# Optimization experiments

Measured on AMD Instinct MI355X. Metric: run time of the kernel, lower is better.

Reference implementation:

```python
import jax, jax.numpy as jnp
import numpy as np

B, S, DQK, DV, H = 4, 2048, 128, 128, 8


def setup_inputs() -> dict:
    key = jax.random.key(0)
    ks = jax.random.split(key, 9)
    s = 0.02
    return {
        "query": jax.random.normal(ks[0], (B, S, DQK), jnp.float32),
        "key": jax.random.normal(ks[1], (B, S, DQK), jnp.float32),
        "value": jax.random.normal(ks[2], (B, S, DV), jnp.float32),
        "WQ": jax.random.normal(ks[3], (DQK, H * DQK), jnp.float32) * s,
        "bQ": jax.random.normal(ks[4], (H * DQK,), jnp.float32) * s,
        "WK": jax.random.normal(ks[5], (DQK, H * DQK), jnp.float32) * s,
        "bK": jax.random.normal(ks[6], (H * DQK,), jnp.float32) * s,
        "WV": jax.random.normal(ks[7], (DV, H * DV), jnp.float32) * s,
        "bV": jax.random.normal(ks[8], (H * DV,), jnp.float32) * s,
    }


def reference(query, key, value, WQ, bQ, WK, bK, WV, bV):
    b, qn, dqk = query.shape
    kn = key.shape[1]
    dv = value.shape[2]
    h = H
    # projections -> [b, n, h, d]
    Q = (query @ WQ + bQ).reshape(b, qn, h, dqk)
    K = (key @ WK + bK).reshape(b, kn, h, dqk)
    V = (value @ WV + bV).reshape(b, kn, h, dv)
    # abs(QK^T)/sqrt(dk) score -- non-standard, prevents flash kernels
    scores = jnp.abs(jnp.einsum("bqhd,bkhd->bhqk", Q, K)) / jnp.sqrt(
        jnp.asarray(dqk, query.dtype)
    )
    w = jax.nn.softmax(scores, axis=-1)  # [b,h,q,k]
    # (complex cast +0j in the original is numerically a no-op on real V)
    out = jnp.einsum("bhqk,bkhd->bqhd", w, V).reshape(b, qn, h * dv)
    return out
```

## Files before the change

kernel.cpp:

```cpp
#include <hip/hip_runtime.h>
#include <hip/hip_bf16.h>

#define B_ 4
#define S_ 2048
#define D_ 128
#define H_ 8

typedef __attribute__((ext_vector_type(8))) short bf16x8;
typedef __attribute__((ext_vector_type(4))) float f32x4;

__device__ __forceinline__ short f2bf(float f) {
  union { float f; unsigned u; } v; v.f = f;
  unsigned u = v.u;
  unsigned r = (u + 0x7FFFu + ((u >> 16) & 1u)) >> 16;
  return (short)r;
}

__device__ __forceinline__ short4 pack4(f32x4 p) {
  union { __hip_bfloat162 h2[2]; short4 s4; } u;
  u.h2[0] = __float22bfloat162_rn(make_float2(p[0], p[1]));
  u.h2[1] = __float22bfloat162_rn(make_float2(p[2], p[3]));
  return u.s4;
}

__device__ __forceinline__ void dma16(const short* g, short* l) {
  __builtin_amdgcn_global_load_lds(
      (const __attribute__((address_space(1))) unsigned int*)g,
      (__attribute__((address_space(3))) unsigned int*)l, 16, 0, 0);
}

__global__ __launch_bounds__(256) void prep(
    const float* __restrict__ WQ, const float* __restrict__ WK, const float* __restrict__ WV,
    short* __restrict__ FQ, short* __restrict__ FK, short* __restrict__ FV) {
  __shared__ float tile[64][65];
  int bw = blockIdx.x >> 5;
  int tl = blockIdx.x & 31;
  int n0 = (tl & 15) * 64, k0 = (tl >> 4) * 64;
  const float* W = (bw == 0) ? WQ : (bw == 1) ? WK : WV;
  short* WF = (bw == 0) ? FQ : (bw == 1) ? FK : FV;
#pragma unroll
  for (int i = 0; i < 16; ++i) {
    int cix = threadIdx.x + 256 * i;
    int rr = cix >> 6, cc = cix & 63;
    tile[rr][cc] = W[(k0 + rr) * 1024 + n0 + cc];
  }
  __syncthreads();
#pragma unroll
  for (int i = 0; i < 16; ++i) {
    int cix = threadIdx.x + 256 * i;
    int rr = cix >> 6, cc = cix & 63;
    int n = n0 + rr, k = k0 + cc;
    size_t off = (size_t)(n >> 7) * 16384
               + (size_t)(((n >> 4) & 7) * 4 + (k >> 5)) * 512
               + ((k >> 3) & 3) * 128 + (n & 15) * 8 + (k & 7);
    WF[off] = f2bf(tile[cc][rr]);
  }
}

template <int MODE>
__device__ __forceinline__ void proj_tile(const float* __restrict__ X,
                                          const short* __restrict__ WF,
                                          const float* __restrict__ bias,
                                          short* __restrict__ out,
                                          int mtile, int ntile,
                                          short* sA) {
  int tid = threadIdx.x;
  int lane = tid & 63, w = tid >> 6;
  int l15 = lane & 15, l4 = lane >> 4;
  int m0 = mtile * 128, n0 = ntile * 128;

#pragma unroll
  for (int j = 0; j < 8; ++j) {
    int f = w * 8 + j;
    const float* src = X + (size_t)(m0 + (f >> 2) * 16 + l15) * 128 + (f & 3) * 32 + l4 * 8;
    float4 v0 = *(const float4*)src;
    float4 v1 = *(const float4*)(src + 4);
    union { struct { short4 lo, hi; } s; bf16x8 v; } u;
    u.s.lo = pack4((f32x4){v0.x, v0.y, v0.z, v0.w});
    u.s.hi = pack4((f32x4){v1.x, v1.y, v1.z, v1.w});
    *(bf16x8*)(sA + f * 512 + lane * 8) = u.v;
  }

  int wr = w >> 1, wc = w & 1;

  const short* wfb = WF + (size_t)ntile * 16384 + wc * 8192 + lane * 8;
  bf16x8 b[16];
#pragma unroll
  for (int q = 0; q < 16; ++q)
    b[q] = *(const bf16x8*)(wfb + q * 512);

  __syncthreads();

  f32x4 acc[4][4];
#pragma unroll
  for (int mi = 0; mi < 4; ++mi)
#pragma unroll
    for (int ni = 0; ni < 4; ++ni) acc[mi][ni] = (f32x4){0.f, 0.f, 0.f, 0.f};

#pragma unroll
  for (int mi = 0; mi < 4; ++mi) {
    bf16x8 a[4];
#pragma unroll
    for (int st = 0; st < 4; ++st)
      a[st] = *(const bf16x8*)(sA + ((wr * 4 + mi) * 4 + st) * 512 + lane * 8);
#pragma unroll
    for (int ni = 0; ni < 4; ++ni) {
#pragma unroll
      for (int st = 0; st < 4; ++st) {
        if (MODE <= 1)
          acc[mi][ni] = __builtin_amdgcn_mfma_f32_16x16x32_bf16(b[ni * 4 + st], a[st], acc[mi][ni], 0, 0, 0);
        else
          acc[mi][ni] = __builtin_amdgcn_mfma_f32_16x16x32_bf16(a[st], b[ni * 4 + st], acc[mi][ni], 0, 0, 0);
      }
    }
  }

  if (MODE == 0) {
#pragma unroll
    for (int mi = 0; mi < 4; ++mi) {
      int sg = m0 + wr * 64 + mi * 16 + l15;
      int bb = sg >> 11, s = sg & 2047;
      short* orow = out + ((size_t)(bb * H_ + ntile) * S_ + s) * D_;
#pragma unroll
      for (int ni = 0; ni < 4; ++ni) {
        int d0 = wc * 64 + ni * 16 + l4 * 4;
        float4 bv = *(const float4*)(bias + n0 + d0);
        f32x4 t = acc[mi][ni];
        t[0] += bv.x; t[1] += bv.y; t[2] += bv.z; t[3] += bv.w;
        *(short4*)(orow + d0) = pack4(t);
      }
    }
  } else if (MODE == 1) {
#pragma unroll
    for (int mi = 0; mi < 4; ++mi) {
      int key = m0 + wr * 64 + mi * 16 + l15;
      int bb = key >> 11, k = key & 2047;
      size_t base = (size_t)(bb * H_ + ntile) * (S_ * D_) + (size_t)(k >> 6) * 8192
                  + ((k >> 4) & 3) * 4 * 512 + (k & 15) * 8;
#pragma unroll
      for (int ni = 0; ni < 4; ++ni) {
        int d0 = wc * 64 + ni * 16 + l4 * 4;
        float4 bv = *(const float4*)(bias + n0 + d0);
        f32x4 t = acc[mi][ni];
        t[0] += bv.x; t[1] += bv.y; t[2] += bv.z; t[3] += bv.w;
        size_t off = base + (size_t)(d0 >> 5) * 512 + ((d0 >> 3) & 3) * 128 + (d0 & 7);
        *(short4*)(out + off) = pack4(t);
      }
    }
  } else {
#pragma unroll
    for (int ni = 0; ni < 4; ++ni) {
      int d = wc * 64 + ni * 16 + l15;
      float bvs = bias[n0 + d];
#pragma unroll
      for (int mi = 0; mi < 4; ++mi) {
        int sg0 = m0 + wr * 64 + mi * 16 + l4 * 4;
        int bb = sg0 >> 11, s0 = sg0 & 2047;
        f32x4 t = acc[mi][ni];
        t[0] += bvs; t[1] += bvs; t[2] += bvs; t[3] += bvs;
        size_t off = (size_t)(bb * H_ + ntile) * (S_ * D_)
                   + (size_t)(s0 >> 6) * 8192
                   + (size_t)((d >> 4) * 2 + ((s0 >> 5) & 1)) * 512
                   + ((s0 >> 3) & 3) * 128 + (d & 15) * 8
                   + (s0 & 7);
        *(short4*)(out + off) = pack4(t);
      }
    }
  }
}

__global__ __launch_bounds__(256, 3) void proj3(
    const float* __restrict__ xq, const float* __restrict__ xk, const float* __restrict__ xv,
    const short* __restrict__ wtq, const short* __restrict__ wtk, const short* __restrict__ wtv,
    const float* __restrict__ bQ, const float* __restrict__ bK, const float* __restrict__ bV,
    short* __restrict__ Qp, short* __restrict__ Kf, short* __restrict__ Vf) {
  __shared__ short sA[16384];
  int work = (blockIdx.x & 7) * 192 + (blockIdx.x >> 3);
  int which = work >> 9;
  int t = work & 511;
  int mtile = t >> 3, ntile = t & 7;
  if (which == 0)      proj_tile<0>(xq, wtq, bQ, Qp, mtile, ntile, sA);
  else if (which == 1) proj_tile<1>(xk, wtk, bK, Kf, mtile, ntile, sA);
  else                 proj_tile<2>(xv, wtv, bV, Vf, mtile, ntile, sA);
}

#define PSTR 72

#define QK_H(KR)                                                               \
  _Pragma("unroll") for (int m = 0; m < 2; ++m) {                              \
    s0[m] = (f32x4){0.f, 0.f, 0.f, 0.f};                                       \
    s1[m] = (f32x4){0.f, 0.f, 0.f, 0.f};                                       \
    _Pragma("unroll") for (int st = 0; st < 4; ++st) {                         \
      s0[m] = __builtin_amdgcn_mfma_f32_16x16x32_bf16(KR[m * 4 + st], aq[0][st], s0[m], 0, 0, 0); \
      s1[m] = __builtin_amdgcn_mfma_f32_16x16x32_bf16(KR[m * 4 + st], aq[1][st], s1[m], 0, 0, 0); \
    }                                                                          \
  }

#define SM_H()                                                                 \
  _Pragma("unroll") for (int m = 0; m < 2; ++m) {                              \
    _Pragma("unroll") for (int r = 0; r < 4; ++r) {                            \
      float p = __builtin_amdgcn_exp2f(fabsf(s0[m][r]) * SC2);                 \
      ls0 += p;                                                                \
      s0[m][r] = p;                                                            \
    }                                                                          \
    *(short4*)(pw + l15 * PSTR + m * 16 + l4 * 4) = pack4(s0[m]);              \
  }                                                                            \
  ap0 = *(const bf16x8*)(pw + l15 * PSTR + l4 * 8);                            \
  _Pragma("unroll") for (int m = 0; m < 2; ++m) {                              \
    _Pragma("unroll") for (int r = 0; r < 4; ++r) {                            \
      float p = __builtin_amdgcn_exp2f(fabsf(s1[m][r]) * SC2);                 \
      ls1 += p;                                                                \
      s1[m][r] = p;                                                            \
    }                                                                          \
    *(short4*)(pw + l15 * PSTR + m * 16 + l4 * 4) = pack4(s1[m]);              \
  }                                                                            \
  ap1 = *(const bf16x8*)(pw + l15 * PSTR + l4 * 8);

#define PV_H()                                                                 \
  _Pragma("unroll") for (int t8 = 0; t8 < 8; ++t8) {                           \
    o0[t8] = __builtin_amdgcn_mfma_f32_16x16x32_bf16(ap0, bv[t8], o0[t8], 0, 0, 0); \
    o1[t8] = __builtin_amdgcn_mfma_f32_16x16x32_bf16(ap1, bv[t8], o1[t8], 0, 0, 0); \
  }

__global__ __launch_bounds__(512, 2) void attn(const short* __restrict__ Qp,
                                               const short* __restrict__ Kf,
                                               const short* __restrict__ Vf,
                                               float* __restrict__ out) {
  __shared__ short sK0[8192], sK1[8192];
  __shared__ short sV0[8192], sV1[8192];
  __shared__ short sP[8 * 16 * PSTR];

  int tid = threadIdx.x;
  int lane = tid & 63, w = tid >> 6;
  int xcd = blockIdx.x & 7;
  int idx = blockIdx.x >> 3;
  int bh  = xcd * 4 + (idx & 3);
  int qt  = idx >> 2;
  int q0  = qt * 256;
  int l15 = lane & 15, l4 = lane >> 4;

  const short* Qbase = Qp + (size_t)bh * S_ * D_;
  const short* kgs = Kf + (size_t)bh * S_ * D_ + 2 * w * 512 + lane * 8;
  const short* vgs = Vf + (size_t)bh * S_ * D_ + 2 * w * 512 + lane * 8;

  dma16(kgs,       sK0 + 2 * w * 512);
  dma16(kgs + 512, sK0 + (2 * w + 1) * 512);
  dma16(vgs,       sV0 + 2 * w * 512);
  dma16(vgs + 512, sV0 + (2 * w + 1) * 512);

  bf16x8 aq[2][4];
#pragma unroll
  for (int g = 0; g < 2; ++g)
#pragma unroll
    for (int st = 0; st < 4; ++st)
      aq[g][st] = *(const bf16x8*)(Qbase + (q0 + w * 32 + g * 16 + l15) * D_ + l4 * 8 + 32 * st);

  f32x4 o0[8], o1[8];
#pragma unroll
  for (int t = 0; t < 8; ++t) {
    o0[t] = (f32x4){0.f, 0.f, 0.f, 0.f};
    o1[t] = (f32x4){0.f, 0.f, 0.f, 0.f};
  }
  float ls0 = 0.f, ls1 = 0.f;

  const float SC2 = 0.127530637f;
  short* pw = sP + w * 16 * PSTR;

  __syncthreads();

  for (int t = 0; t < 32; ++t) {
    const short* sKc = (t & 1) ? sK1 : sK0;
    const short* sVc = (t & 1) ? sV1 : sV0;
    if (t < 31) {
      short* sKn = (t & 1) ? sK0 : sK1;
      short* sVn = (t & 1) ? sV0 : sV1;
      const short* kn = kgs + (size_t)(t + 1) * 8192;
      const short* vn = vgs + (size_t)(t + 1) * 8192;
      dma16(kn,       sKn + 2 * w * 512);
      dma16(kn + 512, sKn + (2 * w + 1) * 512);
      dma16(vn,       sVn + 2 * w * 512);
      dma16(vn + 512, sVn + (2 * w + 1) * 512);
    }
    bf16x8 kA[8], kB[8], bv[8];
#pragma unroll
    for (int j = 0; j < 8; ++j)
      kA[j] = *(const bf16x8*)(sKc + j * 512 + lane * 8);
#pragma unroll
    for (int j = 0; j < 8; ++j)
      kB[j] = *(const bf16x8*)(sKc + 4096 + j * 512 + lane * 8);
#pragma unroll
    for (int j = 0; j < 8; ++j)
      bv[j] = *(const bf16x8*)(sVc + (2 * j) * 512 + lane * 8);
    __builtin_amdgcn_sched_barrier(0);

    f32x4 s0[2], s1[2];
    bf16x8 ap0, ap1;
    __builtin_amdgcn_s_setprio(1);
    QK_H(kA);
    __builtin_amdgcn_s_setprio(0);
    SM_H();
    __builtin_amdgcn_s_setprio(1);
    PV_H();
    __builtin_amdgcn_s_setprio(0);
#pragma unroll
    for (int j = 0; j < 8; ++j)
      bv[j] = *(const bf16x8*)(sVc + (2 * j + 1) * 512 + lane * 8);
    __builtin_amdgcn_s_setprio(1);
    QK_H(kB);
    __builtin_amdgcn_s_setprio(0);
    SM_H();
    __builtin_amdgcn_s_setprio(1);
    PV_H();
    __builtin_amdgcn_s_setprio(0);
    __syncthreads();
  }

  ls0 += __shfl_xor(ls0, 16);
  ls0 += __shfl_xor(ls0, 32);
  ls1 += __shfl_xor(ls1, 16);
  ls1 += __shfl_xor(ls1, 32);
  float inv0[4], inv1[4];
#pragma unroll
  for (int r = 0; r < 4; ++r) {
    inv0[r] = 1.f / __shfl(ls0, l4 * 4 + r);
    inv1[r] = 1.f / __shfl(ls1, l4 * 4 + r);
  }

  int bb = bh >> 3, h = bh & 7;
#pragma unroll
  for (int t = 0; t < 8; ++t) {
#pragma unroll
    for (int r = 0; r < 4; ++r) {
      int qA = q0 + w * 32 + l4 * 4 + r;
      int qB = qA + 16;
      out[((size_t)(bb * S_ + qA)) * (H_ * D_) + h * D_ + t * 16 + l15] = o0[t][r] * inv0[r];
      out[((size_t)(bb * S_ + qB)) * (H_ * D_) + h * D_ + t * 16 + l15] = o1[t][r] * inv1[r];
    }
  }
}

extern "C" void kernel_launch(void* const* d_in, const int* in_sizes, int n_in,
                              void* d_out, int out_size, void* d_ws, size_t ws_size,
                              hipStream_t stream) {
  (void)in_sizes; (void)n_in; (void)out_size; (void)ws_size;
  const float* q  = (const float*)d_in[0];
  const float* k  = (const float*)d_in[1];
  const float* v  = (const float*)d_in[2];
  const float* WQ = (const float*)d_in[3];
  const float* bQ = (const float*)d_in[4];
  const float* WK = (const float*)d_in[5];
  const float* bK = (const float*)d_in[6];
  const float* WV = (const float*)d_in[7];
  const float* bV = (const float*)d_in[8];

  const int NW = D_ * H_ * D_;
  const int NP = B_ * H_ * S_ * D_;

  short* ws  = (short*)d_ws;
  short* wtq = ws;
  short* wtk = wtq + NW;
  short* wtv = wtk + NW;
  short* Qp  = wtv + NW;
  short* Kf  = Qp + NP;
  short* Vf  = Kf + NP;

  prep<<<96, 256, 0, stream>>>(WQ, WK, WV, wtq, wtk, wtv);

  proj3<<<1536, 256, 0, stream>>>(q, k, v, wtq, wtk, wtv, bQ, bK, bV, Qp, Kf, Vf);

  attn<<<256, 512, 0, stream>>>(Qp, Kf, Vf, (float*)d_out);
}
```

Before: 184.0 us.

## Load projection activations directly into registers with prefetch; split P scratch buffers

The projection kernel no longer stages the converted activation tile through shared memory behind a barrier. Each wave loads its own fp32 rows from global memory, converts them to bf16 in registers, and prefetches the next 16-row slice while the current one feeds the MFMAs. The launch-bounds occupancy hint of 3 blocks is removed. In the attention kernel the P scratch is split into two per-wave buffers, so both half-tiles are written before either is read back, which removes the write-read dependency between them at the cost of doubling that LDS allocation.

```diff
diff --git a/kernel.cpp b/kernel.cpp
--- a/kernel.cpp
+++ b/kernel.cpp
@@ -57,31 +57,51 @@
   }
 }
 
+#define PJ_STEP(CUR, NXT, MI, PREF)                                            \
+  {                                                                            \
+    if (PREF) {                                                                \
+      const float* xn = xb + ((MI) + 1) * 2048;                                \
+      _Pragma("unroll") for (int st = 0; st < 4; ++st) {                       \
+        NXT[st][0] = *(const float4*)(xn + st * 32);                           \
+        NXT[st][1] = *(const float4*)(xn + st * 32 + 4);                       \
+      }                                                                        \
+    }                                                                          \
+    bf16x8 a[4];                                                               \
+    _Pragma("unroll") for (int st = 0; st < 4; ++st) {                         \
+      union { struct { short4 lo, hi; } s; bf16x8 v; } u;                      \
+      u.s.lo = pack4((f32x4){CUR[st][0].x, CUR[st][0].y, CUR[st][0].z, CUR[st][0].w}); \
+      u.s.hi = pack4((f32x4){CUR[st][1].x, CUR[st][1].y, CUR[st][1].z, CUR[st][1].w}); \
+      a[st] = u.v;                                                             \
+    }                                                                          \
+    _Pragma("unroll") for (int ni = 0; ni < 4; ++ni) {                         \
+      _Pragma("unroll") for (int st = 0; st < 4; ++st) {                       \
+        if (MODE <= 1)                                                         \
+          acc[MI][ni] = __builtin_amdgcn_mfma_f32_16x16x32_bf16(b[ni * 4 + st], a[st], acc[MI][ni], 0, 0, 0); \
+        else                                                                   \
+          acc[MI][ni] = __builtin_amdgcn_mfma_f32_16x16x32_bf16(a[st], b[ni * 4 + st], acc[MI][ni], 0, 0, 0); \
+      }                                                                        \
+    }                                                                          \
+  }
+
 template <int MODE>
 __device__ __forceinline__ void proj_tile(const float* __restrict__ X,
                                           const short* __restrict__ WF,
                                           const float* __restrict__ bias,
                                           short* __restrict__ out,
-                                          int mtile, int ntile,
-                                          short* sA) {
+                                          int mtile, int ntile) {
   int tid = threadIdx.x;
   int lane = tid & 63, w = tid >> 6;
   int l15 = lane & 15, l4 = lane >> 4;
   int m0 = mtile * 128, n0 = ntile * 128;
-
-#pragma unroll
-  for (int j = 0; j < 8; ++j) {
-    int f = w * 8 + j;
-    const float* src = X + (size_t)(m0 + (f >> 2) * 16 + l15) * 128 + (f & 3) * 32 + l4 * 8;
-    float4 v0 = *(const float4*)src;
-    float4 v1 = *(const float4*)(src + 4);
-    union { struct { short4 lo, hi; } s; bf16x8 v; } u;
-    u.s.lo = pack4((f32x4){v0.x, v0.y, v0.z, v0.w});
-    u.s.hi = pack4((f32x4){v1.x, v1.y, v1.z, v1.w});
-    *(bf16x8*)(sA + f * 512 + lane * 8) = u.v;
-  }
-
   int wr = w >> 1, wc = w & 1;
+
+  const float* xb = X + (size_t)(m0 + wr * 64 + l15) * 128 + l4 * 8;
+  float4 pa[4][2], pb[4][2];
+#pragma unroll
+  for (int st = 0; st < 4; ++st) {
+    pa[st][0] = *(const float4*)(xb + st * 32);
+    pa[st][1] = *(const float4*)(xb + st * 32 + 4);
+  }
 
   const short* wfb = WF + (size_t)ntile * 16384 + wc * 8192 + lane * 8;
   bf16x8 b[16];
@@ -89,31 +109,16 @@
   for (int q = 0; q < 16; ++q)
     b[q] = *(const bf16x8*)(wfb + q * 512);
 
-  __syncthreads();
-
   f32x4 acc[4][4];
 #pragma unroll
   for (int mi = 0; mi < 4; ++mi)
 #pragma unroll
     for (int ni = 0; ni < 4; ++ni) acc[mi][ni] = (f32x4){0.f, 0.f, 0.f, 0.f};
 
-#pragma unroll
-  for (int mi = 0; mi < 4; ++mi) {
-    bf16x8 a[4];
-#pragma unroll
-    for (int st = 0; st < 4; ++st)
-      a[st] = *(const bf16x8*)(sA + ((wr * 4 + mi) * 4 + st) * 512 + lane * 8);
-#pragma unroll
-    for (int ni = 0; ni < 4; ++ni) {
-#pragma unroll
-      for (int st = 0; st < 4; ++st) {
-        if (MODE <= 1)
-          acc[mi][ni] = __builtin_amdgcn_mfma_f32_16x16x32_bf16(b[ni * 4 + st], a[st], acc[mi][ni], 0, 0, 0);
-        else
-          acc[mi][ni] = __builtin_amdgcn_mfma_f32_16x16x32_bf16(a[st], b[ni * 4 + st], acc[mi][ni], 0, 0, 0);
-      }
-    }
-  }
+  PJ_STEP(pa, pb, 0, true);
+  PJ_STEP(pb, pa, 1, true);
+  PJ_STEP(pa, pb, 2, true);
+  PJ_STEP(pb, pa, 3, false);
 
   if (MODE == 0) {
 #pragma unroll
@@ -169,19 +174,18 @@
   }
 }
 
-__global__ __launch_bounds__(256, 3) void proj3(
+__global__ __launch_bounds__(256) void proj3(
     const float* __restrict__ xq, const float* __restrict__ xk, const float* __restrict__ xv,
     const short* __restrict__ wtq, const short* __restrict__ wtk, const short* __restrict__ wtv,
     const float* __restrict__ bQ, const float* __restrict__ bK, const float* __restrict__ bV,
     short* __restrict__ Qp, short* __restrict__ Kf, short* __restrict__ Vf) {
-  __shared__ short sA[16384];
   int work = (blockIdx.x & 7) * 192 + (blockIdx.x >> 3);
   int which = work >> 9;
   int t = work & 511;
   int mtile = t >> 3, ntile = t & 7;
-  if (which == 0)      proj_tile<0>(xq, wtq, bQ, Qp, mtile, ntile, sA);
-  else if (which == 1) proj_tile<1>(xk, wtk, bK, Kf, mtile, ntile, sA);
-  else                 proj_tile<2>(xv, wtv, bV, Vf, mtile, ntile, sA);
+  if (which == 0)      proj_tile<0>(xq, wtq, bQ, Qp, mtile, ntile);
+  else if (which == 1) proj_tile<1>(xk, wtk, bK, Kf, mtile, ntile);
+  else                 proj_tile<2>(xv, wtv, bV, Vf, mtile, ntile);
 }
 
 #define PSTR 72
@@ -203,18 +207,18 @@
       ls0 += p;                                                                \
       s0[m][r] = p;                                                            \
     }                                                                          \
-    *(short4*)(pw + l15 * PSTR + m * 16 + l4 * 4) = pack4(s0[m]);              \
+    *(short4*)(pw0 + l15 * PSTR + m * 16 + l4 * 4) = pack4(s0[m]);             \
   }                                                                            \
-  ap0 = *(const bf16x8*)(pw + l15 * PSTR + l4 * 8);                            \
   _Pragma("unroll") for (int m = 0; m < 2; ++m) {                              \
     _Pragma("unroll") for (int r = 0; r < 4; ++r) {                            \
       float p = __builtin_amdgcn_exp2f(fabsf(s1[m][r]) * SC2);                 \
       ls1 += p;                                                                \
       s1[m][r] = p;                                                            \
     }                                                                          \
-    *(short4*)(pw + l15 * PSTR + m * 16 + l4 * 4) = pack4(s1[m]);              \
+    *(short4*)(pw1 + l15 * PSTR + m * 16 + l4 * 4) = pack4(s1[m]);             \
   }                                                                            \
-  ap1 = *(const bf16x8*)(pw + l15 * PSTR + l4 * 8);
+  ap0 = *(const bf16x8*)(pw0 + l15 * PSTR + l4 * 8);                           \
+  ap1 = *(const bf16x8*)(pw1 + l15 * PSTR + l4 * 8);
 
 #define PV_H()                                                                 \
   _Pragma("unroll") for (int t8 = 0; t8 < 8; ++t8) {                           \
@@ -228,7 +232,7 @@
                                                float* __restrict__ out) {
   __shared__ short sK0[8192], sK1[8192];
   __shared__ short sV0[8192], sV1[8192];
-  __shared__ short sP[8 * 16 * PSTR];
+  __shared__ short sP[16 * 16 * PSTR];
 
   int tid = threadIdx.x;
   int lane = tid & 63, w = tid >> 6;
@@ -264,7 +268,8 @@
   float ls0 = 0.f, ls1 = 0.f;
 
   const float SC2 = 0.127530637f;
-  short* pw = sP + w * 16 * PSTR;
+  short* pw0 = sP + w * 16 * PSTR;
+  short* pw1 = sP + (8 + w) * 16 * PSTR;
 
   __syncthreads();
 
```

New measurement: 191.0 us. 3.8% more time.

## Fuse weight prep, projections and attention into one cooperative kernel

Applied to the files above, without the earlier changes.

Replaces the three launches (weight convert/swizzle, projection GEMM, attention) with a single cooperative kernel of 256 blocks of 512 threads, separated by grid-wide syncs. Each block redoes its share of the projection work as smaller 64-row subtiles processed with 8 waves before running attention. The aim is to remove launch gaps and tail effects between the kernels. In exchange it adds two grid barriers, limits occupancy to one block per CU with a larger shared allocation, and runs the projection phase with a different tiling. It also gives each P-tile half its own shared buffer.

```diff
diff --git a/kernel.cpp b/kernel.cpp
--- a/kernel.cpp
+++ b/kernel.cpp
@@ -1,5 +1,8 @@
 #include <hip/hip_runtime.h>
 #include <hip/hip_bf16.h>
+#include <hip/hip_cooperative_groups.h>
+
+namespace cg = cooperative_groups;
 
 #define B_ 4
 #define S_ 2048
@@ -29,49 +32,20 @@
       (__attribute__((address_space(3))) unsigned int*)l, 16, 0, 0);
 }
 
-__global__ __launch_bounds__(256) void prep(
-    const float* __restrict__ WQ, const float* __restrict__ WK, const float* __restrict__ WV,
-    short* __restrict__ FQ, short* __restrict__ FK, short* __restrict__ FV) {
-  __shared__ float tile[64][65];
-  int bw = blockIdx.x >> 5;
-  int tl = blockIdx.x & 31;
-  int n0 = (tl & 15) * 64, k0 = (tl >> 4) * 64;
-  const float* W = (bw == 0) ? WQ : (bw == 1) ? WK : WV;
-  short* WF = (bw == 0) ? FQ : (bw == 1) ? FK : FV;
-#pragma unroll
-  for (int i = 0; i < 16; ++i) {
-    int cix = threadIdx.x + 256 * i;
-    int rr = cix >> 6, cc = cix & 63;
-    tile[rr][cc] = W[(k0 + rr) * 1024 + n0 + cc];
-  }
-  __syncthreads();
-#pragma unroll
-  for (int i = 0; i < 16; ++i) {
-    int cix = threadIdx.x + 256 * i;
-    int rr = cix >> 6, cc = cix & 63;
-    int n = n0 + rr, k = k0 + cc;
-    size_t off = (size_t)(n >> 7) * 16384
-               + (size_t)(((n >> 4) & 7) * 4 + (k >> 5)) * 512
-               + ((k >> 3) & 3) * 128 + (n & 15) * 8 + (k & 7);
-    WF[off] = f2bf(tile[cc][rr]);
-  }
-}
-
 template <int MODE>
-__device__ __forceinline__ void proj_tile(const float* __restrict__ X,
-                                          const short* __restrict__ WF,
-                                          const float* __restrict__ bias,
-                                          short* __restrict__ out,
-                                          int mtile, int ntile,
-                                          short* sA) {
+__device__ __forceinline__ void proj_tile8(const float* __restrict__ X,
+                                           const short* __restrict__ WF,
+                                           const float* __restrict__ bias,
+                                           short* __restrict__ outp,
+                                           int mtile, int ntile, short* sA) {
   int tid = threadIdx.x;
   int lane = tid & 63, w = tid >> 6;
   int l15 = lane & 15, l4 = lane >> 4;
   int m0 = mtile * 128, n0 = ntile * 128;
 
 #pragma unroll
-  for (int j = 0; j < 8; ++j) {
-    int f = w * 8 + j;
+  for (int j = 0; j < 4; ++j) {
+    int f = w * 4 + j;
     const float* src = X + (size_t)(m0 + (f >> 2) * 16 + l15) * 128 + (f & 3) * 32 + l4 * 8;
     float4 v0 = *(const float4*)src;
     float4 v1 = *(const float4*)(src + 4);
@@ -82,7 +56,6 @@
   }
 
   int wr = w >> 1, wc = w & 1;
-
   const short* wfb = WF + (size_t)ntile * 16384 + wc * 8192 + lane * 8;
   bf16x8 b[16];
 #pragma unroll
@@ -91,18 +64,18 @@
 
   __syncthreads();
 
-  f32x4 acc[4][4];
-#pragma unroll
-  for (int mi = 0; mi < 4; ++mi)
+  f32x4 acc[2][4];
+#pragma unroll
+  for (int mi = 0; mi < 2; ++mi)
 #pragma unroll
     for (int ni = 0; ni < 4; ++ni) acc[mi][ni] = (f32x4){0.f, 0.f, 0.f, 0.f};
 
 #pragma unroll
-  for (int mi = 0; mi < 4; ++mi) {
+  for (int mi = 0; mi < 2; ++mi) {
     bf16x8 a[4];
 #pragma unroll
     for (int st = 0; st < 4; ++st)
-      a[st] = *(const bf16x8*)(sA + ((wr * 4 + mi) * 4 + st) * 512 + lane * 8);
+      a[st] = *(const bf16x8*)(sA + ((wr * 2 + mi) * 4 + st) * 512 + lane * 8);
 #pragma unroll
     for (int ni = 0; ni < 4; ++ni) {
 #pragma unroll
@@ -114,13 +87,14 @@
       }
     }
   }
+  __syncthreads();
 
   if (MODE == 0) {
 #pragma unroll
-    for (int mi = 0; mi < 4; ++mi) {
-      int sg = m0 + wr * 64 + mi * 16 + l15;
-      int bb = sg >> 11, s = sg & 2047;
-      short* orow = out + ((size_t)(bb * H_ + ntile) * S_ + s) * D_;
+    for (int mi = 0; mi < 2; ++mi) {
+      int sg = m0 + wr * 32 + mi * 16 + l15;
+      int b2 = sg >> 11, s = sg & 2047;
+      short* orow = outp + ((size_t)(b2 * H_ + ntile) * S_ + s) * D_;
 #pragma unroll
       for (int ni = 0; ni < 4; ++ni) {
         int d0 = wc * 64 + ni * 16 + l4 * 4;
@@ -132,11 +106,11 @@
     }
   } else if (MODE == 1) {
 #pragma unroll
-    for (int mi = 0; mi < 4; ++mi) {
-      int key = m0 + wr * 64 + mi * 16 + l15;
-      int bb = key >> 11, k = key & 2047;
-      size_t base = (size_t)(bb * H_ + ntile) * (S_ * D_) + (size_t)(k >> 6) * 8192
-                  + ((k >> 4) & 3) * 4 * 512 + (k & 15) * 8;
+    for (int mi = 0; mi < 2; ++mi) {
+      int key = m0 + wr * 32 + mi * 16 + l15;
+      int b2 = key >> 11, kk = key & 2047;
+      size_t base = (size_t)(b2 * H_ + ntile) * (S_ * D_) + (size_t)(kk >> 6) * 8192
+                  + ((kk >> 4) & 3) * 2048 + (kk & 15) * 8;
 #pragma unroll
       for (int ni = 0; ni < 4; ++ni) {
         int d0 = wc * 64 + ni * 16 + l4 * 4;
@@ -144,7 +118,7 @@
         f32x4 t = acc[mi][ni];
         t[0] += bv.x; t[1] += bv.y; t[2] += bv.z; t[3] += bv.w;
         size_t off = base + (size_t)(d0 >> 5) * 512 + ((d0 >> 3) & 3) * 128 + (d0 & 7);
-        *(short4*)(out + off) = pack4(t);
+        *(short4*)(outp + off) = pack4(t);
       }
     }
   } else {
@@ -153,35 +127,20 @@
       int d = wc * 64 + ni * 16 + l15;
       float bvs = bias[n0 + d];
 #pragma unroll
-      for (int mi = 0; mi < 4; ++mi) {
-        int sg0 = m0 + wr * 64 + mi * 16 + l4 * 4;
-        int bb = sg0 >> 11, s0 = sg0 & 2047;
+      for (int mi = 0; mi < 2; ++mi) {
+        int sg0 = m0 + wr * 32 + mi * 16 + l4 * 4;
+        int b2 = sg0 >> 11, s0 = sg0 & 2047;
         f32x4 t = acc[mi][ni];
         t[0] += bvs; t[1] += bvs; t[2] += bvs; t[3] += bvs;
-        size_t off = (size_t)(bb * H_ + ntile) * (S_ * D_)
+        size_t off = (size_t)(b2 * H_ + ntile) * (S_ * D_)
                    + (size_t)(s0 >> 6) * 8192
                    + (size_t)((d >> 4) * 2 + ((s0 >> 5) & 1)) * 512
                    + ((s0 >> 3) & 3) * 128 + (d & 15) * 8
                    + (s0 & 7);
-        *(short4*)(out + off) = pack4(t);
+        *(short4*)(outp + off) = pack4(t);
       }
     }
   }
-}
-
-__global__ __launch_bounds__(256, 3) void proj3(
-    const float* __restrict__ xq, const float* __restrict__ xk, const float* __restrict__ xv,
-    const short* __restrict__ wtq, const short* __restrict__ wtk, const short* __restrict__ wtv,
-    const float* __restrict__ bQ, const float* __restrict__ bK, const float* __restrict__ bV,
-    short* __restrict__ Qp, short* __restrict__ Kf, short* __restrict__ Vf) {
-  __shared__ short sA[16384];
-  int work = (blockIdx.x & 7) * 192 + (blockIdx.x >> 3);
-  int which = work >> 9;
-  int t = work & 511;
-  int mtile = t >> 3, ntile = t & 7;
-  if (which == 0)      proj_tile<0>(xq, wtq, bQ, Qp, mtile, ntile, sA);
-  else if (which == 1) proj_tile<1>(xk, wtk, bK, Kf, mtile, ntile, sA);
-  else                 proj_tile<2>(xv, wtv, bV, Vf, mtile, ntile, sA);
 }
 
 #define PSTR 72
@@ -203,18 +162,18 @@
       ls0 += p;                                                                \
       s0[m][r] = p;                                                            \
     }                                                                          \
-    *(short4*)(pw + l15 * PSTR + m * 16 + l4 * 4) = pack4(s0[m]);              \
+    *(short4*)(pw0 + l15 * PSTR + m * 16 + l4 * 4) = pack4(s0[m]);             \
   }                                                                            \
-  ap0 = *(const bf16x8*)(pw + l15 * PSTR + l4 * 8);                            \
   _Pragma("unroll") for (int m = 0; m < 2; ++m) {                              \
     _Pragma("unroll") for (int r = 0; r < 4; ++r) {                            \
       float p = __builtin_amdgcn_exp2f(fabsf(s1[m][r]) * SC2);                 \
       ls1 += p;                                                                \
       s1[m][r] = p;                                                            \
     }                                                                          \
-    *(short4*)(pw + l15 * PSTR + m * 16 + l4 * 4) = pack4(s1[m]);              \
+    *(short4*)(pw1 + l15 * PSTR + m * 16 + l4 * 4) = pack4(s1[m]);             \
   }                                                                            \
-  ap1 = *(const bf16x8*)(pw + l15 * PSTR + l4 * 8);
+  ap0 = *(const bf16x8*)(pw0 + l15 * PSTR + l4 * 8);                           \
+  ap1 = *(const bf16x8*)(pw1 + l15 * PSTR + l4 * 8);
 
 #define PV_H()                                                                 \
   _Pragma("unroll") for (int t8 = 0; t8 < 8; ++t8) {                           \
@@ -222,22 +181,69 @@
     o1[t8] = __builtin_amdgcn_mfma_f32_16x16x32_bf16(ap1, bv[t8], o1[t8], 0, 0, 0); \
   }
 
-__global__ __launch_bounds__(512, 2) void attn(const short* __restrict__ Qp,
-                                               const short* __restrict__ Kf,
-                                               const short* __restrict__ Vf,
-                                               float* __restrict__ out) {
-  __shared__ short sK0[8192], sK1[8192];
-  __shared__ short sV0[8192], sV1[8192];
-  __shared__ short sP[8 * 16 * PSTR];
+__global__ __launch_bounds__(512, 1) void fused(
+    const float* __restrict__ xq, const float* __restrict__ xk, const float* __restrict__ xv,
+    const float* __restrict__ WQ, const float* __restrict__ WK, const float* __restrict__ WV,
+    const float* __restrict__ bQ, const float* __restrict__ bK, const float* __restrict__ bV,
+    short* __restrict__ wfq, short* __restrict__ wfk, short* __restrict__ wfv,
+    short* __restrict__ Qp, short* __restrict__ Kf, short* __restrict__ Vf,
+    float* __restrict__ out) {
+  __shared__ short smem[51200];
 
   int tid = threadIdx.x;
   int lane = tid & 63, w = tid >> 6;
+  int l15 = lane & 15, l4 = lane >> 4;
   int xcd = blockIdx.x & 7;
   int idx = blockIdx.x >> 3;
   int bh  = xcd * 4 + (idx & 3);
   int qt  = idx >> 2;
-  int q0  = qt * 256;
-  int l15 = lane & 15, l4 = lane >> 4;
+  int bb  = bh >> 3, h = bh & 7;
+
+  if (blockIdx.x < 96) {
+    float* tile = (float*)smem;
+    int bw = blockIdx.x >> 5, tl = blockIdx.x & 31;
+    int n0 = (tl & 15) * 64, k0 = (tl >> 4) * 64;
+    const float* W = (bw == 0) ? WQ : (bw == 1) ? WK : WV;
+    short* WF = (bw == 0) ? wfq : (bw == 1) ? wfk : wfv;
+#pragma unroll
+    for (int i = 0; i < 8; ++i) {
+      int cix = tid + 512 * i;
+      int rr = cix >> 6, cc = cix & 63;
+      tile[rr * 65 + cc] = W[(k0 + rr) * 1024 + n0 + cc];
+    }
+    __syncthreads();
+#pragma unroll
+    for (int i = 0; i < 8; ++i) {
+      int cix = tid + 512 * i;
+      int rr = cix >> 6, cc = cix & 63;
+      int n = n0 + rr, k = k0 + cc;
+      size_t off = (size_t)(n >> 7) * 16384
+                 + (size_t)(((n >> 4) & 7) * 4 + (k >> 5)) * 512
+                 + ((k >> 3) & 3) * 128 + (n & 15) * 8 + (k & 7);
+      WF[off] = f2bf(tile[cc * 65 + rr]);
+    }
+  }
+  cg::this_grid().sync();
+
+  {
+    short* sA = smem;
+    int mt0 = bb * 16 + qt * 2;
+    proj_tile8<0>(xq, wfq, bQ, Qp, mt0,     h, sA);
+    proj_tile8<0>(xq, wfq, bQ, Qp, mt0 + 1, h, sA);
+    proj_tile8<1>(xk, wfk, bK, Kf, mt0,     h, sA);
+    proj_tile8<1>(xk, wfk, bK, Kf, mt0 + 1, h, sA);
+    proj_tile8<2>(xv, wfv, bV, Vf, mt0,     h, sA);
+    proj_tile8<2>(xv, wfv, bV, Vf, mt0 + 1, h, sA);
+  }
+  cg::this_grid().sync();
+
+  short* sK0 = smem;
+  short* sK1 = smem + 8192;
+  short* sV0 = smem + 16384;
+  short* sV1 = smem + 24576;
+  short* sP  = smem + 32768;
+
+  int q0 = qt * 256;
 
   const short* Qbase = Qp + (size_t)bh * S_ * D_;
   const short* kgs = Kf + (size_t)bh * S_ * D_ + 2 * w * 512 + lane * 8;
@@ -264,7 +270,8 @@
   float ls0 = 0.f, ls1 = 0.f;
 
   const float SC2 = 0.127530637f;
-  short* pw = sP + w * 16 * PSTR;
+  short* pw0 = sP + w * 16 * PSTR;
+  short* pw1 = sP + (8 + w) * 16 * PSTR;
 
   __syncthreads();
 
@@ -326,7 +333,6 @@
     inv1[r] = 1.f / __shfl(ls1, l4 * 4 + r);
   }
 
-  int bb = bh >> 3, h = bh & 7;
 #pragma unroll
   for (int t = 0; t < 8; ++t) {
 #pragma unroll
@@ -357,16 +363,21 @@
   const int NP = B_ * H_ * S_ * D_;
 
   short* ws  = (short*)d_ws;
-  short* wtq = ws;
-  short* wtk = wtq + NW;
-  short* wtv = wtk + NW;
-  short* Qp  = wtv + NW;
+  short* wfq = ws;
+  short* wfk = wfq + NW;
+  short* wfv = wfk + NW;
+  short* Qp  = wfv + NW;
   short* Kf  = Qp + NP;
   short* Vf  = Kf + NP;
-
-  prep<<<96, 256, 0, stream>>>(WQ, WK, WV, wtq, wtk, wtv);
-
-  proj3<<<1536, 256, 0, stream>>>(q, k, v, wtq, wtk, wtv, bQ, bK, bV, Qp, Kf, Vf);
-
-  attn<<<256, 512, 0, stream>>>(Qp, Kf, Vf, (float*)d_out);
-}
+  float* outp = (float*)d_out;
+
+  void* args[] = {
+    (void*)&q, (void*)&k, (void*)&v,
+    (void*)&WQ, (void*)&WK, (void*)&WV,
+    (void*)&bQ, (void*)&bK, (void*)&bV,
+    (void*)&wfq, (void*)&wfk, (void*)&wfv,
+    (void*)&Qp, (void*)&Kf, (void*)&Vf,
+    (void*)&outp,
+  };
+  hipLaunchCooperativeKernel((void*)fused, dim3(256), dim3(512), args, 0, stream);
+}
```

Result: slower. 254.7 us (+38.5%).

## Compute two output column tiles per projection block and double-buffer P scratch

Applied to the files above, without the earlier changes.

Each projection block now loads and converts one 128-row input tile, keeps its A fragments in registers, and computes two adjacent 128-column output tiles. This halves the grid and the redundant fp32 input loads and bf16 conversions, at the cost of more registers held per thread. In the attention kernel, the two 16-row P tiles per wave now get separate LDS scratch regions. Both tiles are written before either is read back, removing the write-read dependency between them, at the cost of doubling the sP LDS footprint.

```diff
diff --git a/kernel.cpp b/kernel.cpp
--- a/kernel.cpp
+++ b/kernel.cpp
@@ -58,16 +58,15 @@
 }
 
 template <int MODE>
-__device__ __forceinline__ void proj_tile(const float* __restrict__ X,
+__device__ __forceinline__ void proj_pair(const float* __restrict__ X,
                                           const short* __restrict__ WF,
                                           const float* __restrict__ bias,
                                           short* __restrict__ out,
-                                          int mtile, int ntile,
-                                          short* sA) {
+                                          int mtile, int np, short* sA) {
   int tid = threadIdx.x;
   int lane = tid & 63, w = tid >> 6;
   int l15 = lane & 15, l4 = lane >> 4;
-  int m0 = mtile * 128, n0 = ntile * 128;
+  int m0 = mtile * 128;
 
 #pragma unroll
   for (int j = 0; j < 8; ++j) {
@@ -83,87 +82,96 @@
 
   int wr = w >> 1, wc = w & 1;
 
-  const short* wfb = WF + (size_t)ntile * 16384 + wc * 8192 + lane * 8;
-  bf16x8 b[16];
-#pragma unroll
-  for (int q = 0; q < 16; ++q)
-    b[q] = *(const bf16x8*)(wfb + q * 512);
-
   __syncthreads();
 
-  f32x4 acc[4][4];
+  bf16x8 a[4][4];
 #pragma unroll
   for (int mi = 0; mi < 4; ++mi)
 #pragma unroll
-    for (int ni = 0; ni < 4; ++ni) acc[mi][ni] = (f32x4){0.f, 0.f, 0.f, 0.f};
-
-#pragma unroll
-  for (int mi = 0; mi < 4; ++mi) {
-    bf16x8 a[4];
-#pragma unroll
     for (int st = 0; st < 4; ++st)
-      a[st] = *(const bf16x8*)(sA + ((wr * 4 + mi) * 4 + st) * 512 + lane * 8);
-#pragma unroll
-    for (int ni = 0; ni < 4; ++ni) {
-#pragma unroll
-      for (int st = 0; st < 4; ++st) {
-        if (MODE <= 1)
-          acc[mi][ni] = __builtin_amdgcn_mfma_f32_16x16x32_bf16(b[ni * 4 + st], a[st], acc[mi][ni], 0, 0, 0);
-        else
-          acc[mi][ni] = __builtin_amdgcn_mfma_f32_16x16x32_bf16(a[st], b[ni * 4 + st], acc[mi][ni], 0, 0, 0);
+      a[mi][st] = *(const bf16x8*)(sA + ((wr * 4 + mi) * 4 + st) * 512 + lane * 8);
+
+#pragma unroll
+  for (int nt = 0; nt < 2; ++nt) {
+    int ntile = np * 2 + nt;
+    int n0 = ntile * 128;
+
+    const short* wfb = WF + (size_t)ntile * 16384 + wc * 8192 + lane * 8;
+    bf16x8 b[16];
+#pragma unroll
+    for (int q = 0; q < 16; ++q)
+      b[q] = *(const bf16x8*)(wfb + q * 512);
+
+    f32x4 acc[4][4];
+#pragma unroll
+    for (int mi = 0; mi < 4; ++mi)
+#pragma unroll
+      for (int ni = 0; ni < 4; ++ni) acc[mi][ni] = (f32x4){0.f, 0.f, 0.f, 0.f};
+
+#pragma unroll
+    for (int mi = 0; mi < 4; ++mi) {
+#pragma unroll
+      for (int ni = 0; ni < 4; ++ni) {
+#pragma unroll
+        for (int st = 0; st < 4; ++st) {
+          if (MODE <= 1)
+            acc[mi][ni] = __builtin_amdgcn_mfma_f32_16x16x32_bf16(b[ni * 4 + st], a[mi][st], acc[mi][ni], 0, 0, 0);
+          else
+            acc[mi][ni] = __builtin_amdgcn_mfma_f32_16x16x32_bf16(a[mi][st], b[ni * 4 + st], acc[mi][ni], 0, 0, 0);
+        }
       }
     }
-  }
-
-  if (MODE == 0) {
-#pragma unroll
-    for (int mi = 0; mi < 4; ++mi) {
-      int sg = m0 + wr * 64 + mi * 16 + l15;
-      int bb = sg >> 11, s = sg & 2047;
-      short* orow = out + ((size_t)(bb * H_ + ntile) * S_ + s) * D_;
+
+    if (MODE == 0) {
+#pragma unroll
+      for (int mi = 0; mi < 4; ++mi) {
+        int sg = m0 + wr * 64 + mi * 16 + l15;
+        int bb = sg >> 11, s = sg & 2047;
+        short* orow = out + ((size_t)(bb * H_ + ntile) * S_ + s) * D_;
+#pragma unroll
+        for (int ni = 0; ni < 4; ++ni) {
+          int d0 = wc * 64 + ni * 16 + l4 * 4;
+          float4 bv = *(const float4*)(bias + n0 + d0);
+          f32x4 t = acc[mi][ni];
+          t[0] += bv.x; t[1] += bv.y; t[2] += bv.z; t[3] += bv.w;
+          *(short4*)(orow + d0) = pack4(t);
+        }
+      }
+    } else if (MODE == 1) {
+#pragma unroll
+      for (int mi = 0; mi < 4; ++mi) {
+        int key = m0 + wr * 64 + mi * 16 + l15;
+        int bb = key >> 11, kk = key & 2047;
+        size_t base = (size_t)(bb * H_ + ntile) * (S_ * D_) + (size_t)(kk >> 6) * 8192
+                    + ((kk >> 4) & 3) * 2048 + (kk & 15) * 8;
+#pragma unroll
+        for (int ni = 0; ni < 4; ++ni) {
+          int d0 = wc * 64 + ni * 16 + l4 * 4;
+          float4 bv = *(const float4*)(bias + n0 + d0);
+          f32x4 t = acc[mi][ni];
+          t[0] += bv.x; t[1] += bv.y; t[2] += bv.z; t[3] += bv.w;
+          size_t off = base + (size_t)(d0 >> 5) * 512 + ((d0 >> 3) & 3) * 128 + (d0 & 7);
+          *(short4*)(out + off) = pack4(t);
+        }
+      }
+    } else {
 #pragma unroll
       for (int ni = 0; ni < 4; ++ni) {
-        int d0 = wc * 64 + ni * 16 + l4 * 4;
-        float4 bv = *(const float4*)(bias + n0 + d0);
-        f32x4 t = acc[mi][ni];
-        t[0] += bv.x; t[1] += bv.y; t[2] += bv.z; t[3] += bv.w;
-        *(short4*)(orow + d0) = pack4(t);
-      }
-    }
-  } else if (MODE == 1) {
-#pragma unroll
-    for (int mi = 0; mi < 4; ++mi) {
-      int key = m0 + wr * 64 + mi * 16 + l15;
-      int bb = key >> 11, k = key & 2047;
-      size_t base = (size_t)(bb * H_ + ntile) * (S_ * D_) + (size_t)(k >> 6) * 8192
-                  + ((k >> 4) & 3) * 4 * 512 + (k & 15) * 8;
-#pragma unroll
-      for (int ni = 0; ni < 4; ++ni) {
-        int d0 = wc * 64 + ni * 16 + l4 * 4;
-        float4 bv = *(const float4*)(bias + n0 + d0);
-        f32x4 t = acc[mi][ni];
-        t[0] += bv.x; t[1] += bv.y; t[2] += bv.z; t[3] += bv.w;
-        size_t off = base + (size_t)(d0 >> 5) * 512 + ((d0 >> 3) & 3) * 128 + (d0 & 7);
-        *(short4*)(out + off) = pack4(t);
-      }
-    }
-  } else {
-#pragma unroll
-    for (int ni = 0; ni < 4; ++ni) {
-      int d = wc * 64 + ni * 16 + l15;
-      float bvs = bias[n0 + d];
-#pragma unroll
-      for (int mi = 0; mi < 4; ++mi) {
-        int sg0 = m0 + wr * 64 + mi * 16 + l4 * 4;
-        int bb = sg0 >> 11, s0 = sg0 & 2047;
-        f32x4 t = acc[mi][ni];
-        t[0] += bvs; t[1] += bvs; t[2] += bvs; t[3] += bvs;
-        size_t off = (size_t)(bb * H_ + ntile) * (S_ * D_)
-                   + (size_t)(s0 >> 6) * 8192
-                   + (size_t)((d >> 4) * 2 + ((s0 >> 5) & 1)) * 512
-                   + ((s0 >> 3) & 3) * 128 + (d & 15) * 8
-                   + (s0 & 7);
-        *(short4*)(out + off) = pack4(t);
+        int d = wc * 64 + ni * 16 + l15;
+        float bvs = bias[n0 + d];
+#pragma unroll
+        for (int mi = 0; mi < 4; ++mi) {
+          int sg0 = m0 + wr * 64 + mi * 16 + l4 * 4;
+          int bb = sg0 >> 11, s0 = sg0 & 2047;
+          f32x4 t = acc[mi][ni];
+          t[0] += bvs; t[1] += bvs; t[2] += bvs; t[3] += bvs;
+          size_t off = (size_t)(bb * H_ + ntile) * (S_ * D_)
+                     + (size_t)(s0 >> 6) * 8192
+                     + (size_t)((d >> 4) * 2 + ((s0 >> 5) & 1)) * 512
+                     + ((s0 >> 3) & 3) * 128 + (d & 15) * 8
+                     + (s0 & 7);
+          *(short4*)(out + off) = pack4(t);
+        }
       }
     }
   }
@@ -175,13 +183,13 @@
     const float* __restrict__ bQ, const float* __restrict__ bK, const float* __restrict__ bV,
     short* __restrict__ Qp, short* __restrict__ Kf, short* __restrict__ Vf) {
   __shared__ short sA[16384];
-  int work = (blockIdx.x & 7) * 192 + (blockIdx.x >> 3);
-  int which = work >> 9;
-  int t = work & 511;
-  int mtile = t >> 3, ntile = t & 7;
-  if (which == 0)      proj_tile<0>(xq, wtq, bQ, Qp, mtile, ntile, sA);
-  else if (which == 1) proj_tile<1>(xk, wtk, bK, Kf, mtile, ntile, sA);
-  else                 proj_tile<2>(xv, wtv, bV, Vf, mtile, ntile, sA);
+  int work = (blockIdx.x & 7) * 96 + (blockIdx.x >> 3);
+  int which = work >> 8;
+  int t = work & 255;
+  int mtile = t >> 2, np = t & 3;
+  if (which == 0)      proj_pair<0>(xq, wtq, bQ, Qp, mtile, np, sA);
+  else if (which == 1) proj_pair<1>(xk, wtk, bK, Kf, mtile, np, sA);
+  else                 proj_pair<2>(xv, wtv, bV, Vf, mtile, np, sA);
 }
 
 #define PSTR 72
@@ -203,18 +211,18 @@
       ls0 += p;                                                                \
       s0[m][r] = p;                                                            \
     }                                                                          \
-    *(short4*)(pw + l15 * PSTR + m * 16 + l4 * 4) = pack4(s0[m]);              \
+    *(short4*)(pw0 + l15 * PSTR + m * 16 + l4 * 4) = pack4(s0[m]);             \
   }                                                                            \
-  ap0 = *(const bf16x8*)(pw + l15 * PSTR + l4 * 8);                            \
   _Pragma("unroll") for (int m = 0; m < 2; ++m) {                              \
     _Pragma("unroll") for (int r = 0; r < 4; ++r) {                            \
       float p = __builtin_amdgcn_exp2f(fabsf(s1[m][r]) * SC2);                 \
       ls1 += p;                                                                \
       s1[m][r] = p;                                                            \
     }                                                                          \
-    *(short4*)(pw + l15 * PSTR + m * 16 + l4 * 4) = pack4(s1[m]);              \
+    *(short4*)(pw1 + l15 * PSTR + m * 16 + l4 * 4) = pack4(s1[m]);             \
   }                                                                            \
-  ap1 = *(const bf16x8*)(pw + l15 * PSTR + l4 * 8);
+  ap0 = *(const bf16x8*)(pw0 + l15 * PSTR + l4 * 8);                           \
+  ap1 = *(const bf16x8*)(pw1 + l15 * PSTR + l4 * 8);
 
 #define PV_H()                                                                 \
   _Pragma("unroll") for (int t8 = 0; t8 < 8; ++t8) {                           \
@@ -228,7 +236,7 @@
                                                float* __restrict__ out) {
   __shared__ short sK0[8192], sK1[8192];
   __shared__ short sV0[8192], sV1[8192];
-  __shared__ short sP[8 * 16 * PSTR];
+  __shared__ short sP[16 * 16 * PSTR];
 
   int tid = threadIdx.x;
   int lane = tid & 63, w = tid >> 6;
@@ -264,7 +272,8 @@
   float ls0 = 0.f, ls1 = 0.f;
 
   const float SC2 = 0.127530637f;
-  short* pw = sP + w * 16 * PSTR;
+  short* pw0 = sP + w * 16 * PSTR;
+  short* pw1 = sP + (8 + w) * 16 * PSTR;
 
   __syncthreads();
 
@@ -366,7 +375,7 @@
 
   prep<<<96, 256, 0, stream>>>(WQ, WK, WV, wtq, wtk, wtv);
 
-  proj3<<<1536, 256, 0, stream>>>(q, k, v, wtq, wtk, wtv, bQ, bK, bV, Qp, Kf, Vf);
+  proj3<<<768, 256, 0, stream>>>(q, k, v, wtq, wtk, wtv, bQ, bK, bV, Qp, Kf, Vf);
 
   attn<<<256, 512, 0, stream>>>(Qp, Kf, Vf, (float*)d_out);
 }
```

Measured after the change: 184.9 us. No clear change (+0.5%).
